# Kernel tuning notes

Hardware: AMD Instinct MI355X
Metric: run time of the kernel (lower is better)

Reference implementation:

```python
import jax, jax.numpy as jnp
import numpy as np

B, H = 16384, 64          # batch, human_num
SELF_DIM, HUMAN_DIM = 6, 7
D = 32                    # gcn2_w1_dim / embedding dim


def _lin(key, fin, fout):
    return jax.random.normal(key, (fin, fout), jnp.float32) / np.sqrt(fin)


def setup_inputs() -> dict:
    key = jax.random.key(0)
    ks = jax.random.split(key, 40)
    inp = {}
    inp["state"] = jax.random.normal(ks[0], (B, H, SELF_DIM + HUMAN_DIM), jnp.float32)
    inp["dropout"] = 0
    # w_r: mlp(6 -> 64 -> 32, last_relu=True)
    inp["wr_w1"] = _lin(ks[1], SELF_DIM, 64); inp["wr_b1"] = jnp.zeros(64, jnp.float32)
    inp["wr_w2"] = _lin(ks[2], 64, D);        inp["wr_b2"] = jnp.zeros(D, jnp.float32)
    # w_h: mlp(7 -> 64 -> 32, last_relu=True)
    inp["wh_w1"] = _lin(ks[3], HUMAN_DIM, 64); inp["wh_b1"] = jnp.zeros(64, jnp.float32)
    inp["wh_w2"] = _lin(ks[4], 64, D);         inp["wh_b2"] = jnp.zeros(D, jnp.float32)
    # hetero GraphConv weights: per edge type (rh: robot->human, hr: human->robot, hh: human->human),
    # per layer. GraphConv: out = lin_rel(scatter_sum(x_src)) + lin_root(x_dst); lin_root has no bias.
    i = 5
    for L in (1, 2):
        for et in ("rh", "hr", "hh"):
            inp[f"rel_{et}{L}"] = _lin(ks[i], D, D); i += 1
            inp[f"brel_{et}{L}"] = jnp.zeros(D, jnp.float32)
            inp[f"root_{et}{L}"] = _lin(ks[i], D, D); i += 1
    # value_net: mlp(32 -> 150 -> 100 -> 1), no last relu
    inp["vn_w1"] = _lin(ks[i], D, 150);  inp["vn_b1"] = jnp.zeros(150, jnp.float32); i += 1
    inp["vn_w2"] = _lin(ks[i], 150, 100); inp["vn_b2"] = jnp.zeros(100, jnp.float32); i += 1
    inp["vn_w3"] = _lin(ks[i], 100, 1);  inp["vn_b3"] = jnp.zeros(1, jnp.float32)
    return inp


def _hetero_layer(r, h, rel_rh, brel_rh, root_rh, rel_hr, brel_hr, root_hr,
                  rel_hh, brel_hh, root_hh):
    # r: [B, D] robot nodes; h: [B, H, D] human nodes
    sum_h = h.sum(axis=1)  # [B, D]
    # robot receives scatter-sum over all humans (star graph, one robot target)
    new_r = jax.nn.relu(sum_h @ rel_hr + brel_hr + r @ root_hr)
    # each human receives: robot message + sum of all OTHER humans (full graph minus self-loops)
    agg_hh = sum_h[:, None, :] - h  # [B, H, D]
    new_h = jax.nn.relu((r @ rel_rh)[:, None, :] + brel_rh
                        + agg_hh @ rel_hh + brel_hh
                        + h @ root_rh + h @ root_hh)
    return new_r, new_h


def _forward(state, wr_w1, wr_b1, wr_w2, wr_b2, wh_w1, wh_b1, wh_w2, wh_b2,
             rel_rh1, brel_rh1, root_rh1, rel_hr1, brel_hr1, root_hr1,
             rel_hh1, brel_hh1, root_hh1,
             rel_rh2, brel_rh2, root_rh2, rel_hr2, brel_hr2, root_hr2,
             rel_hh2, brel_hh2, root_hh2,
             vn_w1, vn_b1, vn_w2, vn_b2, vn_w3, vn_b3):
    self_state = state[:, 0, :SELF_DIM]        # [B, 6]
    human_states = state[:, :, SELF_DIM:]      # [B, H, 7]
    r = jax.nn.relu(jax.nn.relu(self_state @ wr_w1 + wr_b1) @ wr_w2 + wr_b2)      # [B, D]
    h = jax.nn.relu(jax.nn.relu(human_states @ wh_w1 + wh_b1) @ wh_w2 + wh_b2)    # [B, H, D]
    r, h = _hetero_layer(r, h, rel_rh1, brel_rh1, root_rh1, rel_hr1, brel_hr1,
                         root_hr1, rel_hh1, brel_hh1, root_hh1)
    r, h = _hetero_layer(r, h, rel_rh2, brel_rh2, root_rh2, rel_hr2, brel_hr2,
                         root_hr2, rel_hh2, brel_hh2, root_hh2)
    v = jax.nn.relu(r @ vn_w1 + vn_b1)
    v = jax.nn.relu(v @ vn_w2 + vn_b2)
    return v @ vn_w3 + vn_b3                    # [B, 1]


def reference(state, dropout, wr_w1, wr_b1, wr_w2, wr_b2, wh_w1, wh_b1, wh_w2, wh_b2,
              rel_rh1, brel_rh1, root_rh1, rel_hr1, brel_hr1, root_hr1,
              rel_hh1, brel_hh1, root_hh1,
              rel_rh2, brel_rh2, root_rh2, rel_hr2, brel_hr2, root_hr2,
              rel_hh2, brel_hh2, root_hh2,
              vn_w1, vn_b1, vn_w2, vn_b2, vn_w3, vn_b3):
    # dropout is accepted but unused (matches the torch forward signature)
    return _forward(state, wr_w1, wr_b1, wr_w2, wr_b2, wh_w1, wh_b1, wh_w2, wh_b2,
                    rel_rh1, brel_rh1, root_rh1, rel_hr1, brel_hr1, root_hr1,
                    rel_hh1, brel_hh1, root_hh1,
                    rel_rh2, brel_rh2, root_rh2, rel_hr2, brel_hr2, root_hr2,
                    rel_hh2, brel_hh2, root_hh2,
                    vn_w1, vn_b1, vn_w2, vn_b2, vn_w3, vn_b3)
```

## Files before the change

kernel.cpp:

```cpp
#include <hip/hip_runtime.h>

#define BTOT 16384

typedef __attribute__((ext_vector_type(8))) short bf16x8;
typedef __attribute__((ext_vector_type(4))) float f32x4;

#define MFMA16(a,b,c) __builtin_amdgcn_mfma_f32_16x16x32_bf16((a),(b),(c),0,0,0)

#if __has_builtin(__builtin_amdgcn_cvt_pk_bf16_f32)
typedef __attribute__((ext_vector_type(2))) __bf16 hwbf2;
static __device__ __forceinline__ unsigned pk2(float a, float b) {
    hwbf2 v = __builtin_amdgcn_cvt_pk_bf16_f32(a, b);
    return __builtin_bit_cast(unsigned, v);
}
#else
static __device__ __forceinline__ unsigned pk2(float a, float b) {
    unsigned ua = __float_as_uint(a), ub = __float_as_uint(b);
    unsigned ra = (ua + 0x7FFFu + ((ua >> 16) & 1u)) >> 16;
    unsigned rb = (ub + 0x7FFFu + ((ub >> 16) & 1u)) >> 16;
    return (ra & 0xFFFFu) | (rb << 16);
}
#endif
static __device__ __forceinline__ unsigned short bfhi(float x) {
    return (unsigned short)(pk2(x, 0.f) & 0xFFFFu);
}
static __device__ __forceinline__ float b2f(unsigned short h) {
    return __uint_as_float(((unsigned)h) << 16);
}
static __device__ __forceinline__ short f2s(float x) { return (short)bfhi(x); }
static __device__ __forceinline__ unsigned short bfhi_m(float x) {
    unsigned u = __float_as_uint(x);
    return (unsigned short)((u + 0x7FFFu + ((u >> 16) & 1u)) >> 16);
}
static __device__ __forceinline__ unsigned short bflo_m(float x) {
    unsigned short h = bfhi_m(x);
    return bfhi_m(x - b2f(h));
}
static __device__ __forceinline__ bf16x8 zero8() {
    bf16x8 v;
    #pragma unroll
    for (int i = 0; i < 8; ++i) v[i] = 0;
    return v;
}

__global__ void pack_frags(
    const float* __restrict__ wh_w1, const float* __restrict__ wh_b1,
    const float* __restrict__ wh_w2,
    const float* __restrict__ root_rh1, const float* __restrict__ root_hh1,
    const float* __restrict__ rel_hh1,
    const float* __restrict__ wr_w2,
    const float* __restrict__ rel_hr1, const float* __restrict__ root_hr1,
    const float* __restrict__ rel_rh1,
    const float* __restrict__ rel_hr2, const float* __restrict__ root_hr2,
    const float* __restrict__ vn_w1, const float* __restrict__ vn_w2,
    const float* __restrict__ brel_hr1, const float* __restrict__ brel_rh1,
    const float* __restrict__ brel_hh1, const float* __restrict__ brel_hr2,
    short* __restrict__ pk)
{
    int t = blockIdx.x * blockDim.x + threadIdx.x;
    if (t < 52736) {
        int f = t >> 9, r = t & 511;
        int lane = r >> 3, j = r & 7;
        int q = lane >> 4, c = lane & 15;
        int k = q * 8 + j;
        unsigned short outv;
        if (f < 4) {
            int m = f * 16 + c;
            float v = (k < 7) ? wh_w1[k * 64 + m] : (k == 7 ? wh_b1[m] : 0.f);
            outv = bfhi_m(v);
        } else if (f < 8) {
            int u = f - 4, ks = u >> 1, nt = u & 1;
            int kr = ks * 32 + (j >> 2) * 16 + q * 4 + (j & 3);
            outv = bfhi_m(wh_w2[kr * 32 + nt * 16 + c]);
        } else if (f < 10) {
            int n = (f - 8) * 16 + c;
            int ko = (k >> 1) + ((k & 1) << 4);
            outv = bfhi_m(root_rh1[ko * 32 + n] + root_hh1[ko * 32 + n] - rel_hh1[ko * 32 + n]);
        } else if (f < 22) {
            int u = f - 10, ks = u >> 1, nt = u & 1;
            int kp = ks * 32 + k;
            float w = wr_w2[(kp & 63) * 32 + nt * 16 + c];
            outv = (kp < 128) ? bfhi_m(w) : bflo_m(w);
        } else if (f < 46) {
            int u = f - 22, ks = u >> 2, nt = u & 3;
            int kp = ks * 32 + k, seg = kp >> 5, kk = kp & 31;
            int n2 = (nt & 1) * 16 + c;
            bool sPart = (seg < 2) || (seg == 4);
            const float* W = (nt < 2) ? (sPart ? rel_hr1 : root_hr1)
                                      : (sPart ? rel_hh1 : rel_rh1);
            float w = W[kk * 32 + n2];
            outv = (seg < 4) ? bfhi_m(w) : bflo_m(w);
        } else if (f < 58) {
            int u = f - 46, ks = u >> 1, nt = u & 1;
            int kp = ks * 32 + k, seg = kp >> 5, kk = kp & 31;
            int n = nt * 16 + c;
            bool sPart = (seg < 2) || (seg == 4);
            const float* W = sPart ? rel_hr2 : root_hr2;
            float w = W[kk * 32 + n];
            outv = (seg < 4) ? bfhi_m(w) : bflo_m(w);
        } else if (f < 68) {
            int n = (f - 58) * 16 + c;
            outv = (n < 150) ? bfhi_m(vn_w1[k * 150 + n]) : 0;
        } else {
            int u = f - 68, kt = u / 7, nt = u - kt * 7;
            int kk = kt * 32 + k, n = nt * 16 + c;
            outv = (kk < 150 && n < 100) ? bfhi_m(vn_w2[kk * 100 + n]) : 0;
        }
        pk[t] = (short)outv;
    } else if (t < 52800) {
        int i = t - 52736;
        float* bp = (float*)(pk + 52736);
        bp[i] = (i < 32) ? brel_hr1[i] : brel_rh1[i - 32] + brel_hh1[i - 32];
    } else if (t < 52832) {
        int i = t - 52800;
        float* bp = (float*)(pk + 52864);
        bp[i] = brel_hr2[i];
    }
}

__global__ __launch_bounds__(256) void fused_main(
    const float* __restrict__ state, const short* __restrict__ pk,
    const float* __restrict__ wr_w1, const float* __restrict__ wr_b1,
    const float* __restrict__ wr_b2, const float* __restrict__ wh_b2,
    short* __restrict__ r2buf)
{
    __shared__ __align__(16) short wbuf[4][4096];

    const int tid = threadIdx.x;
    const int wv = tid >> 6, lane = tid & 63;
    const int q = lane >> 4, c = lane & 15;
    const int b = blockIdx.x * 4 + wv;
    const float* st = state + (size_t)b * 832;
    short* T = wbuf[wv];

    const bf16x8* pk16 = (const bf16x8*)pk;
    const float* bg1f = (const float*)(pk + 52736);
    const float* bg2f = (const float*)(pk + 52864);
    const f32x4 z4 = {0.f, 0.f, 0.f, 0.f};

    bf16x8 A1[4], Bh2v[4], Bev[2];
    #pragma unroll
    for (int i = 0; i < 4; ++i) A1[i] = pk16[i * 64 + lane];
    #pragma unroll
    for (int i = 0; i < 4; ++i) Bh2v[i] = pk16[(4 + i) * 64 + lane];
    #pragma unroll
    for (int i = 0; i < 2; ++i) Bev[i] = pk16[(8 + i) * 64 + lane];

    {
        float hf[7];
        #pragma unroll
        for (int m = 0; m < 7; ++m) hf[m] = st[lane * 13 + 6 + m];
        uint4 v = make_uint4(pk2(hf[0], hf[1]), pk2(hf[2], hf[3]),
                             pk2(hf[4], hf[5]), pk2(hf[6], 1.0f));
        *(uint4*)(T + lane * 8) = v;
    }

    float trh;
    {
        float acc = wr_b1[lane];
        #pragma unroll
        for (int m = 0; m < 6; ++m) acc = fmaf(st[m], wr_w1[m * 64 + lane], acc);
        trh = fmaxf(acc, 0.f);
    }

    asm volatile("s_waitcnt lgkmcnt(0)" ::: "memory");

    bf16x8 bx[4];
    #pragma unroll
    for (int ht = 0; ht < 4; ++ht) {
        bf16x8 v = zero8();
        if (q == 0) v = *(const bf16x8*)(T + (ht * 16 + c) * 8);
        bx[ht] = v;
    }

    #pragma unroll
    for (int mhp = 0; mhp < 2; ++mhp) {
        #pragma unroll
        for (int ht = 0; ht < 4; ++ht) {
            f32x4 d0 = MFMA16(A1[2 * mhp + 0], bx[ht], z4);
            f32x4 d1 = MFMA16(A1[2 * mhp + 1], bx[ht], z4);
            d0 = __builtin_elementwise_max(d0, z4);
            d1 = __builtin_elementwise_max(d1, z4);
            uint4 w = make_uint4(pk2(d0[0], d0[1]), pk2(d0[2], d0[3]),
                                 pk2(d1[0], d1[1]), pk2(d1[2], d1[3]));
            int row = ht * 16 + c;
            int p = (mhp * 4 + q) ^ (c & 7);
            *(uint4*)(T + row * 64 + p * 8) = w;
        }
    }

    asm volatile("s_waitcnt lgkmcnt(0)" ::: "memory");

    const float b2a = wh_b2[c], b2b = wh_b2[16 + c];
    const f32x4 b2a4 = {b2a, b2a, b2a, b2a}, b2b4 = {b2b, b2b, b2b, b2b};
    f32x4 psv0 = z4, psv1 = z4;
    #pragma unroll
    for (int mt = 0; mt < 4; ++mt) {
        int row = mt * 16 + c;
        bf16x8 a0 = *(const bf16x8*)(T + row * 64 + ((q ^ (c & 7))) * 8);
        bf16x8 a1 = *(const bf16x8*)(T + row * 64 + (((q + 4) ^ (c & 7))) * 8);
        f32x4 e0 = MFMA16(a0, Bh2v[0], z4); e0 = MFMA16(a1, Bh2v[2], e0);
        f32x4 e1 = MFMA16(a0, Bh2v[1], z4); e1 = MFMA16(a1, Bh2v[3], e1);
        e0 = __builtin_elementwise_max(e0 + b2a4, z4);
        e1 = __builtin_elementwise_max(e1 + b2b4, z4);
        psv0 += e0; psv1 += e1;
        #pragma unroll
        for (int r = 0; r < 4; ++r) {
            int hrow = mt * 16 + q * 4 + r;
            *(unsigned*)(T + hrow * 32 + (((c >> 2) ^ r)) * 8 + (c & 3) * 2) = pk2(e0[r], e1[r]);
        }
    }
    float ps0 = (psv0[0] + psv0[1]) + (psv0[2] + psv0[3]);
    float ps1 = (psv1[0] + psv1[1]) + (psv1[2] + psv1[3]);
    ps0 += __shfl_xor(ps0, 16); ps0 += __shfl_xor(ps0, 32);
    ps1 += __shfl_xor(ps1, 16); ps1 += __shfl_xor(ps1, 32);

    {
        short* SB = T + 3712;
        if (q == 0) {
            unsigned short h0 = bfhi(ps0), h1 = bfhi(ps1);
            SB[c] = (short)h0;        SB[16 + c] = (short)h1;
            SB[32 + c] = (short)bfhi(ps0 - b2f(h0));
            SB[48 + c] = (short)bfhi(ps1 - b2f(h1));
            SB[128 + c] = (short)h0;  SB[144 + c] = (short)h1;
        }
        short* TR = T + 3904;
        unsigned short th = bfhi(trh);
        TR[lane] = (short)th;
        TR[64 + lane] = (short)bfhi(trh - b2f(th));
        TR[128 + lane] = (short)th;
    }
    __syncthreads();

    if (wv == 0) {
        bf16x8 art[6];
        #pragma unroll
        for (int ks = 0; ks < 6; ++ks) {
            bf16x8 v = zero8();
            if (c < 4) v = *(const bf16x8*)(wbuf[c] + 3904 + ks * 32 + q * 8);
            art[ks] = v;
        }
        f32x4 dr0 = z4, dr1 = z4;
        #pragma unroll
        for (int ks = 0; ks < 6; ++ks) {
            dr0 = MFMA16(art[ks], pk16[(10 + ks * 2 + 0) * 64 + lane], dr0);
            dr1 = MFMA16(art[ks], pk16[(10 + ks * 2 + 1) * 64 + lane], dr1);
        }
        const float wb0 = wr_b2[c], wb1 = wr_b2[16 + c];
        if (q == 0) {
            #pragma unroll
            for (int r = 0; r < 4; ++r) {
                float v0 = fmaxf(dr0[r] + wb0, 0.f), v1 = fmaxf(dr1[r] + wb1, 0.f);
                short* SBr = wbuf[r] + 3712;
                unsigned short h0 = bfhi(v0), h1 = bfhi(v1);
                SBr[64 + c] = (short)h0;  SBr[96 + c]  = (short)bfhi(v0 - b2f(h0));  SBr[160 + c] = (short)h0;
                SBr[80 + c] = (short)h1;  SBr[112 + c] = (short)bfhi(v1 - b2f(h1));  SBr[176 + c] = (short)h1;
            }
        }
        asm volatile("s_waitcnt lgkmcnt(0)" ::: "memory");

        bf16x8 ag[6];
        #pragma unroll
        for (int ks = 0; ks < 6; ++ks) {
            bf16x8 v = zero8();
            if (c < 4) v = *(const bf16x8*)(wbuf[c] + 3712 + ks * 32 + q * 8);
            ag[ks] = v;
        }
        f32x4 dg[4] = {z4, z4, z4, z4};
        #pragma unroll
        for (int ks = 0; ks < 6; ++ks) {
            #pragma unroll
            for (int nt = 0; nt < 4; ++nt)
                dg[nt] = MFMA16(ag[ks], pk16[(22 + ks * 4 + nt) * 64 + lane], dg[nt]);
        }
        if (q == 0) {
            #pragma unroll
            for (int nt = 0; nt < 2; ++nt) {
                float bias = bg1f[nt * 16 + c];
                #pragma unroll
                for (int r = 0; r < 4; ++r) {
                    float v = fmaxf(dg[nt][r] + bias, 0.f);
                    short* G2r = wbuf[r] + 3520;
                    unsigned short hh = bfhi(v);
                    G2r[64 + nt * 16 + c]  = (short)hh;
                    G2r[96 + nt * 16 + c]  = (short)bfhi(v - b2f(hh));
                    G2r[160 + nt * 16 + c] = (short)hh;
                }
            }
            #pragma unroll
            for (int nt = 2; nt < 4; ++nt) {
                float bias = bg1f[nt * 16 + c];
                #pragma unroll
                for (int r = 0; r < 4; ++r)
                    ((float*)(wbuf[r] + 3456))[(nt - 2) * 16 + c] = dg[nt][r] + bias;
            }
        }
    }
    __syncthreads();

    {
        const float* C1 = (const float*)(T + 3456);
        const float c10 = C1[c], c11 = C1[16 + c];
        const f32x4 c10v = {c10, c10, c10, c10}, c11v = {c11, c11, c11, c11};
        f32x4 acc0 = z4, acc1 = z4;
        #pragma unroll
        for (int mt = 0; mt < 4; ++mt) {
            int row = mt * 16 + c;
            bf16x8 ah = *(const bf16x8*)(T + row * 32 + ((q ^ (c & 3))) * 8);
            f32x4 g0 = MFMA16(ah, Bev[0], z4);
            f32x4 g1 = MFMA16(ah, Bev[1], z4);
            acc0 += __builtin_elementwise_max(g0 + c10v, z4);
            acc1 += __builtin_elementwise_max(g1 + c11v, z4);
        }
        float t0 = (acc0[0] + acc0[1]) + (acc0[2] + acc0[3]);
        float t1 = (acc1[0] + acc1[1]) + (acc1[2] + acc1[3]);
        t0 += __shfl_xor(t0, 16); t0 += __shfl_xor(t0, 32);
        t1 += __shfl_xor(t1, 16); t1 += __shfl_xor(t1, 32);
        short* G2 = T + 3520;
        if (q == 0) {
            unsigned short h0 = bfhi(t0), h1 = bfhi(t1);
            G2[c] = (short)h0;        G2[16 + c] = (short)h1;
            G2[32 + c] = (short)bfhi(t0 - b2f(h0));
            G2[48 + c] = (short)bfhi(t1 - b2f(h1));
            G2[128 + c] = (short)h0;  G2[144 + c] = (short)h1;
        }
    }
    __syncthreads();

    if (wv == 0) {
        bf16x8 a2[6];
        #pragma unroll
        for (int ks = 0; ks < 6; ++ks) {
            bf16x8 v = zero8();
            if (c < 4) v = *(const bf16x8*)(wbuf[c] + 3520 + ks * 32 + q * 8);
            a2[ks] = v;
        }
        f32x4 d0 = z4, d1 = z4;
        #pragma unroll
        for (int ks = 0; ks < 6; ++ks) {
            d0 = MFMA16(a2[ks], pk16[(46 + ks * 2 + 0) * 64 + lane], d0);
            d1 = MFMA16(a2[ks], pk16[(46 + ks * 2 + 1) * 64 + lane], d1);
        }
        if (q == 0) {
            const int b0 = blockIdx.x * 4;
            const float g0 = bg2f[c], g1 = bg2f[16 + c];
            #pragma unroll
            for (int r = 0; r < 4; ++r) {
                r2buf[(b0 + r) * 32 + c]      = f2s(fmaxf(d0[r] + g0, 0.f));
                r2buf[(b0 + r) * 32 + 16 + c] = f2s(fmaxf(d1[r] + g1, 0.f));
            }
        }
    }
}

__global__ __launch_bounds__(256) void head_kernel(
    const short* __restrict__ pk,
    const float* __restrict__ vn_b1, const float* __restrict__ vn_b2,
    const float* __restrict__ vn_w3, const float* __restrict__ vn_b3,
    float* __restrict__ out)
{
    __shared__ __align__(16) short sh_v1[4][16 * 168];
    const int wv = threadIdx.x >> 6, lane = threadIdx.x & 63;
    const int q = lane >> 4, c = lane & 15;
    const int tile = blockIdx.x * 4 + wv;
    const bf16x8* wf = (const bf16x8*)pk;
    const short* r2b = pk + 53248;
    const f32x4 z4 = {0.f, 0.f, 0.f, 0.f};

    bf16x8 a1 = *(const bf16x8*)&r2b[(tile * 16 + c) * 32 + q * 8];
    short* vb = sh_v1[wv];
    #pragma unroll
    for (int nt = 0; nt < 10; ++nt) {
        f32x4 d = MFMA16(a1, wf[(58 + nt) * 64 + lane], z4);
        int n = nt * 16 + c;
        float bias = (n < 150) ? vn_b1[n] : 0.f;
        #pragma unroll
        for (int r = 0; r < 4; ++r) {
            float v = (n < 150) ? fmaxf(d[r] + bias, 0.f) : 0.f;
            vb[(q * 4 + r) * 168 + n] = f2s(v);
        }
    }
    __syncthreads();

    bf16x8 a2[5];
    #pragma unroll
    for (int kt = 0; kt < 5; ++kt)
        a2[kt] = *(const bf16x8*)&vb[c * 168 + kt * 32 + q * 8];

    float racc[4] = {0.f, 0.f, 0.f, 0.f};
    #pragma unroll
    for (int nt = 0; nt < 7; ++nt) {
        f32x4 d = z4;
        #pragma unroll
        for (int kt = 0; kt < 5; ++kt)
            d = MFMA16(a2[kt], wf[(68 + kt * 7 + nt) * 64 + lane], d);
        int n = nt * 16 + c;
        float bias = (n < 100) ? vn_b2[n] : 0.f;
        float w3   = (n < 100) ? vn_w3[n] : 0.f;
        #pragma unroll
        for (int r = 0; r < 4; ++r) racc[r] += fmaxf(d[r] + bias, 0.f) * w3;
    }
    #pragma unroll
    for (int m = 1; m < 16; m <<= 1) {
        #pragma unroll
        for (int r = 0; r < 4; ++r) racc[r] += __shfl_xor(racc[r], m);
    }
    if (c == 0) {
        float b3 = vn_b3[0];
        #pragma unroll
        for (int r = 0; r < 4; ++r) out[tile * 16 + q * 4 + r] = racc[r] + b3;
    }
}

extern "C" void kernel_launch(void* const* d_in, const int* in_sizes, int n_in,
                              void* d_out, int out_size, void* d_ws, size_t ws_size,
                              hipStream_t stream) {
    const float* state    = (const float*)d_in[0];
    const float* wr_w1    = (const float*)d_in[2];
    const float* wr_b1    = (const float*)d_in[3];
    const float* wr_w2    = (const float*)d_in[4];
    const float* wr_b2    = (const float*)d_in[5];
    const float* wh_w1    = (const float*)d_in[6];
    const float* wh_b1    = (const float*)d_in[7];
    const float* wh_w2    = (const float*)d_in[8];
    const float* wh_b2    = (const float*)d_in[9];
    const float* rel_rh1  = (const float*)d_in[10];
    const float* brel_rh1 = (const float*)d_in[11];
    const float* root_rh1 = (const float*)d_in[12];
    const float* rel_hr1  = (const float*)d_in[13];
    const float* brel_hr1 = (const float*)d_in[14];
    const float* root_hr1 = (const float*)d_in[15];
    const float* rel_hh1  = (const float*)d_in[16];
    const float* brel_hh1 = (const float*)d_in[17];
    const float* root_hh1 = (const float*)d_in[18];
    const float* rel_hr2  = (const float*)d_in[22];
    const float* brel_hr2 = (const float*)d_in[23];
    const float* root_hr2 = (const float*)d_in[24];
    const float* vn_w1    = (const float*)d_in[28];
    const float* vn_b1    = (const float*)d_in[29];
    const float* vn_w2    = (const float*)d_in[30];
    const float* vn_b2    = (const float*)d_in[31];
    const float* vn_w3    = (const float*)d_in[32];
    const float* vn_b3    = (const float*)d_in[33];
    float* out = (float*)d_out;
    short* pk  = (short*)d_ws;
    short* r2buf = pk + 53248;

    pack_frags<<<207, 256, 0, stream>>>(wh_w1, wh_b1, wh_w2,
                                        root_rh1, root_hh1, rel_hh1, wr_w2,
                                        rel_hr1, root_hr1, rel_rh1,
                                        rel_hr2, root_hr2, vn_w1, vn_w2,
                                        brel_hr1, brel_rh1, brel_hh1, brel_hr2, pk);
    fused_main<<<BTOT / 4, 256, 0, stream>>>(state, pk, wr_w1, wr_b1, wr_b2, wh_b2, r2buf);
    head_kernel<<<BTOT / 64, 256, 0, stream>>>(pk, vn_b1, vn_b2, vn_w3, vn_b3, out);
}
```

Before: 183.0 us.

## Compute per-block robot GEMMs redundantly in all waves to drop barrier and wave-0 serialization

Previously wave 0 alone ran the small robot-side MFMA GEMMs for the four batch rows and shared the results through LDS behind an extra __syncthreads, leaving the other waves idle. Now every wave computes these GEMMs redundantly. Each wave reads the robot features from a compact per-wave LDS layout and picks its own row with a shuffle, which removes one block barrier and the cross-wave LDS handoff of the layer-1 constants. The cost is extra MFMA issue in every wave and some reindexing of the LDS layout, with a correctness risk if per-wave rows or offsets are mismatched.

```diff
diff --git a/kernel.cpp b/kernel.cpp
--- a/kernel.cpp
+++ b/kernel.cpp
@@ -222,85 +222,81 @@
             SB[c] = (short)h0;        SB[16 + c] = (short)h1;
             SB[32 + c] = (short)bfhi(ps0 - b2f(h0));
             SB[48 + c] = (short)bfhi(ps1 - b2f(h1));
-            SB[128 + c] = (short)h0;  SB[144 + c] = (short)h1;
-        }
-        short* TR = T + 3904;
+        }
+        short* TR = T + 3840;
         unsigned short th = bfhi(trh);
         TR[lane] = (short)th;
         TR[64 + lane] = (short)bfhi(trh - b2f(th));
-        TR[128 + lane] = (short)th;
     }
     __syncthreads();
 
-    if (wv == 0) {
-        bf16x8 art[6];
-        #pragma unroll
-        for (int ks = 0; ks < 6; ++ks) {
-            bf16x8 v = zero8();
-            if (c < 4) v = *(const bf16x8*)(wbuf[c] + 3904 + ks * 32 + q * 8);
-            art[ks] = v;
-        }
-        f32x4 dr0 = z4, dr1 = z4;
-        #pragma unroll
-        for (int ks = 0; ks < 6; ++ks) {
-            dr0 = MFMA16(art[ks], pk16[(10 + ks * 2 + 0) * 64 + lane], dr0);
-            dr1 = MFMA16(art[ks], pk16[(10 + ks * 2 + 1) * 64 + lane], dr1);
-        }
+    const short* rowS = wbuf[c & 3];
+
+    bf16x8 at0 = *(const bf16x8*)(rowS + 3840 + q * 8);
+    bf16x8 at1 = *(const bf16x8*)(rowS + 3872 + q * 8);
+    bf16x8 at2 = *(const bf16x8*)(rowS + 3904 + q * 8);
+    bf16x8 at3 = *(const bf16x8*)(rowS + 3936 + q * 8);
+    f32x4 dr0 = z4, dr1 = z4;
+    dr0 = MFMA16(at0, pk16[10 * 64 + lane], dr0); dr1 = MFMA16(at0, pk16[11 * 64 + lane], dr1);
+    dr0 = MFMA16(at1, pk16[12 * 64 + lane], dr0); dr1 = MFMA16(at1, pk16[13 * 64 + lane], dr1);
+    dr0 = MFMA16(at2, pk16[14 * 64 + lane], dr0); dr1 = MFMA16(at2, pk16[15 * 64 + lane], dr1);
+    dr0 = MFMA16(at3, pk16[16 * 64 + lane], dr0); dr1 = MFMA16(at3, pk16[17 * 64 + lane], dr1);
+    dr0 = MFMA16(at0, pk16[18 * 64 + lane], dr0); dr1 = MFMA16(at0, pk16[19 * 64 + lane], dr1);
+    dr0 = MFMA16(at1, pk16[20 * 64 + lane], dr0); dr1 = MFMA16(at1, pk16[21 * 64 + lane], dr1);
+
+    {
         const float wb0 = wr_b2[c], wb1 = wr_b2[16 + c];
         if (q == 0) {
             #pragma unroll
             for (int r = 0; r < 4; ++r) {
                 float v0 = fmaxf(dr0[r] + wb0, 0.f), v1 = fmaxf(dr1[r] + wb1, 0.f);
-                short* SBr = wbuf[r] + 3712;
                 unsigned short h0 = bfhi(v0), h1 = bfhi(v1);
-                SBr[64 + c] = (short)h0;  SBr[96 + c]  = (short)bfhi(v0 - b2f(h0));  SBr[160 + c] = (short)h0;
-                SBr[80 + c] = (short)h1;  SBr[112 + c] = (short)bfhi(v1 - b2f(h1));  SBr[176 + c] = (short)h1;
+                T[2048 + r * 32 + c]      = (short)h0;
+                T[2048 + r * 32 + 16 + c] = (short)h1;
+                T[2176 + r * 32 + c]      = (short)bfhi(v0 - b2f(h0));
+                T[2176 + r * 32 + 16 + c] = (short)bfhi(v1 - b2f(h1));
             }
         }
-        asm volatile("s_waitcnt lgkmcnt(0)" ::: "memory");
-
-        bf16x8 ag[6];
-        #pragma unroll
-        for (int ks = 0; ks < 6; ++ks) {
-            bf16x8 v = zero8();
-            if (c < 4) v = *(const bf16x8*)(wbuf[c] + 3712 + ks * 32 + q * 8);
-            ag[ks] = v;
-        }
-        f32x4 dg[4] = {z4, z4, z4, z4};
-        #pragma unroll
-        for (int ks = 0; ks < 6; ++ks) {
+    }
+    asm volatile("s_waitcnt lgkmcnt(0)" ::: "memory");
+
+    bf16x8 as0 = *(const bf16x8*)(rowS + 3712 + q * 8);
+    bf16x8 as1 = *(const bf16x8*)(rowS + 3744 + q * 8);
+    bf16x8 ar0 = *(const bf16x8*)(T + 2048 + (c & 3) * 32 + q * 8);
+    bf16x8 ar1 = *(const bf16x8*)(T + 2176 + (c & 3) * 32 + q * 8);
+    f32x4 dg[4] = {z4, z4, z4, z4};
+    #pragma unroll
+    for (int nt = 0; nt < 4; ++nt) dg[nt] = MFMA16(as0, pk16[(22 +  0 + nt) * 64 + lane], dg[nt]);
+    #pragma unroll
+    for (int nt = 0; nt < 4; ++nt) dg[nt] = MFMA16(as1, pk16[(22 +  4 + nt) * 64 + lane], dg[nt]);
+    #pragma unroll
+    for (int nt = 0; nt < 4; ++nt) dg[nt] = MFMA16(ar0, pk16[(22 +  8 + nt) * 64 + lane], dg[nt]);
+    #pragma unroll
+    for (int nt = 0; nt < 4; ++nt) dg[nt] = MFMA16(ar1, pk16[(22 + 12 + nt) * 64 + lane], dg[nt]);
+    #pragma unroll
+    for (int nt = 0; nt < 4; ++nt) dg[nt] = MFMA16(as0, pk16[(22 + 16 + nt) * 64 + lane], dg[nt]);
+    #pragma unroll
+    for (int nt = 0; nt < 4; ++nt) dg[nt] = MFMA16(ar0, pk16[(22 + 20 + nt) * 64 + lane], dg[nt]);
+
+    const float c10 = __shfl(dg[2][wv], c) + bg1f[32 + c];
+    const float c11 = __shfl(dg[3][wv], c) + bg1f[48 + c];
+
+    {
+        if (q == 0) {
+            const float gb0 = bg1f[c], gb1 = bg1f[16 + c];
             #pragma unroll
-            for (int nt = 0; nt < 4; ++nt)
-                dg[nt] = MFMA16(ag[ks], pk16[(22 + ks * 4 + nt) * 64 + lane], dg[nt]);
-        }
-        if (q == 0) {
-            #pragma unroll
-            for (int nt = 0; nt < 2; ++nt) {
-                float bias = bg1f[nt * 16 + c];
-                #pragma unroll
-                for (int r = 0; r < 4; ++r) {
-                    float v = fmaxf(dg[nt][r] + bias, 0.f);
-                    short* G2r = wbuf[r] + 3520;
-                    unsigned short hh = bfhi(v);
-                    G2r[64 + nt * 16 + c]  = (short)hh;
-                    G2r[96 + nt * 16 + c]  = (short)bfhi(v - b2f(hh));
-                    G2r[160 + nt * 16 + c] = (short)hh;
-                }
+            for (int r = 0; r < 4; ++r) {
+                float v0 = fmaxf(dg[0][r] + gb0, 0.f), v1 = fmaxf(dg[1][r] + gb1, 0.f);
+                unsigned short h0 = bfhi(v0), h1 = bfhi(v1);
+                T[2304 + r * 32 + c]      = (short)h0;
+                T[2304 + r * 32 + 16 + c] = (short)h1;
+                T[2432 + r * 32 + c]      = (short)bfhi(v0 - b2f(h0));
+                T[2432 + r * 32 + 16 + c] = (short)bfhi(v1 - b2f(h1));
             }
-            #pragma unroll
-            for (int nt = 2; nt < 4; ++nt) {
-                float bias = bg1f[nt * 16 + c];
-                #pragma unroll
-                for (int r = 0; r < 4; ++r)
-                    ((float*)(wbuf[r] + 3456))[(nt - 2) * 16 + c] = dg[nt][r] + bias;
-            }
-        }
-    }
-    __syncthreads();
-
-    {
-        const float* C1 = (const float*)(T + 3456);
-        const float c10 = C1[c], c11 = C1[16 + c];
+        }
+    }
+
+    {
         const f32x4 c10v = {c10, c10, c10, c10}, c11v = {c11, c11, c11, c11};
         f32x4 acc0 = z4, acc1 = z4;
         #pragma unroll
@@ -322,33 +318,26 @@
             G2[c] = (short)h0;        G2[16 + c] = (short)h1;
             G2[32 + c] = (short)bfhi(t0 - b2f(h0));
             G2[48 + c] = (short)bfhi(t1 - b2f(h1));
-            G2[128 + c] = (short)h0;  G2[144 + c] = (short)h1;
         }
     }
     __syncthreads();
 
-    if (wv == 0) {
-        bf16x8 a2[6];
-        #pragma unroll
-        for (int ks = 0; ks < 6; ++ks) {
-            bf16x8 v = zero8();
-            if (c < 4) v = *(const bf16x8*)(wbuf[c] + 3520 + ks * 32 + q * 8);
-            a2[ks] = v;
-        }
+    {
+        bf16x8 ag0 = *(const bf16x8*)(rowS + 3520 + q * 8);
+        bf16x8 ag1 = *(const bf16x8*)(rowS + 3552 + q * 8);
+        bf16x8 agr0 = *(const bf16x8*)(T + 2304 + (c & 3) * 32 + q * 8);
+        bf16x8 agr1 = *(const bf16x8*)(T + 2432 + (c & 3) * 32 + q * 8);
         f32x4 d0 = z4, d1 = z4;
-        #pragma unroll
-        for (int ks = 0; ks < 6; ++ks) {
-            d0 = MFMA16(a2[ks], pk16[(46 + ks * 2 + 0) * 64 + lane], d0);
-            d1 = MFMA16(a2[ks], pk16[(46 + ks * 2 + 1) * 64 + lane], d1);
-        }
+        d0 = MFMA16(ag0,  pk16[46 * 64 + lane], d0); d1 = MFMA16(ag0,  pk16[47 * 64 + lane], d1);
+        d0 = MFMA16(ag1,  pk16[48 * 64 + lane], d0); d1 = MFMA16(ag1,  pk16[49 * 64 + lane], d1);
+        d0 = MFMA16(agr0, pk16[50 * 64 + lane], d0); d1 = MFMA16(agr0, pk16[51 * 64 + lane], d1);
+        d0 = MFMA16(agr1, pk16[52 * 64 + lane], d0); d1 = MFMA16(agr1, pk16[53 * 64 + lane], d1);
+        d0 = MFMA16(ag0,  pk16[54 * 64 + lane], d0); d1 = MFMA16(ag0,  pk16[55 * 64 + lane], d1);
+        d0 = MFMA16(agr0, pk16[56 * 64 + lane], d0); d1 = MFMA16(agr0, pk16[57 * 64 + lane], d1);
         if (q == 0) {
-            const int b0 = blockIdx.x * 4;
             const float g0 = bg2f[c], g1 = bg2f[16 + c];
-            #pragma unroll
-            for (int r = 0; r < 4; ++r) {
-                r2buf[(b0 + r) * 32 + c]      = f2s(fmaxf(d0[r] + g0, 0.f));
-                r2buf[(b0 + r) * 32 + 16 + c] = f2s(fmaxf(d1[r] + g1, 0.f));
-            }
+            r2buf[b * 32 + c]      = f2s(fmaxf(d0[wv] + g0, 0.f));
+            r2buf[b * 32 + 16 + c] = f2s(fmaxf(d1[wv] + g1, 0.f));
         }
     }
 }
```

Result: slower. 188.1 us (+2.8%).
